# Optimization experiments

Hardware: AMD Instinct MI355X
Metric: run time of the kernel (lower is better)

Reference implementation:

```python
import jax, jax.numpy as jnp
import numpy as np

N = 131072       # total nodes (B graphs x P nodes)
P = 4096         # nodes per graph
B = 32           # graphs in batch
E = 2097152      # edges (avg degree 16)
IN_DIM = 64
HID = 128
OUT = 16
EPS = 1e-5
SLOPE = 0.01


def _degrees(idx):
    # structural degree, clamped to min 1 (as DGL GraphConv does)
    d = jax.ops.segment_sum(jnp.ones((E,), jnp.float32), idx, num_segments=N)
    return jnp.maximum(d, 1.0)


def _graph_conv(x, W, src, dst, ew):
    # DGL GraphConv, norm='both', bias=False, with scalar edge weights:
    # h = D_out^{-1/2} x ; m_v = sum_{(u->v)} w_e h_u ; out = (D_in^{-1/2} m) W
    h = x * jax.lax.rsqrt(_degrees(src))[:, None]
    m = jax.ops.segment_sum(ew[:, None] * h[src], dst, num_segments=N)  # [N, F]
    return (m * jax.lax.rsqrt(_degrees(dst))[:, None]) @ W


def _graph_norm(x, gamma, beta, alpha):
    # GraphNorm (Cai et al. / PyG, batch=None): stats over all nodes per feature
    mu = jnp.mean(x, axis=0)
    c = x - alpha * mu
    var = jnp.mean(c * c, axis=0)
    return c * jax.lax.rsqrt(var + EPS) * gamma + beta


def _mean_nodes(h, gid):
    # per-graph mean readout; every graph has exactly P nodes
    return jax.ops.segment_sum(h, gid, num_segments=B) / P


def setup_inputs() -> dict:
    key = jax.random.key(0)
    ks = jax.random.split(key, 8)
    src = jax.random.randint(ks[0], (E,), 0, N, dtype=jnp.int32)
    # keep edges within each 4096-node graph block (batched DGL graph)
    dst = (src // P) * P + jax.random.randint(ks[1], (E,), 0, P, dtype=jnp.int32)
    features = jax.random.normal(ks[2], (N, IN_DIM), jnp.float32)
    edge_weights = jax.random.uniform(ks[3], (E,), jnp.float32)
    # kaiming/xavier-scale init approximations
    W1 = jax.random.normal(ks[4], (IN_DIM, HID), jnp.float32) * np.sqrt(2.0 / IN_DIM)
    W2 = jax.random.normal(ks[5], (HID, HID), jnp.float32) * np.sqrt(2.0 / HID)
    Wc = jax.random.normal(ks[6], (OUT, 2 * HID), jnp.float32) * np.sqrt(1.0 / (2 * HID))
    ones = jnp.ones((HID,), jnp.float32)
    zeros = jnp.zeros((HID,), jnp.float32)
    return {
        'features': features, 'edge_weights': edge_weights, 'src': src, 'dst': dst,
        'W1': W1, 'W2': W2, 'Wc': Wc,
        'gamma1': ones, 'beta1': zeros, 'alpha1': ones,
        'gamma2': ones, 'beta2': zeros, 'alpha2': ones,
    }


def reference(features, edge_weights, src, dst, W1, W2, Wc,
              gamma1, beta1, alpha1, gamma2, beta2, alpha2):
    gid = jnp.arange(N, dtype=jnp.int32) // P  # node -> graph id
    h1 = _graph_conv(features, W1, src, dst, edge_weights)
    h1 = jax.nn.leaky_relu(_graph_norm(h1, gamma1, beta1, alpha1), SLOPE)
    r1 = _mean_nodes(h1, gid)                  # [B, HID]
    h2 = _graph_conv(h1, W2, src, dst, edge_weights)
    h2 = jax.nn.leaky_relu(_graph_norm(h2, gamma2, beta2, alpha2), SLOPE)
    r2 = _mean_nodes(h2, gid)                  # [B, HID]
    readouts = jnp.concatenate([r1, r2], axis=1)  # [B, 2*HID]
    return readouts @ Wc.T                     # [B, OUT]
```

## Files before the change

### kernel.cpp

```cpp
#include <hip/hip_runtime.h>
#include <hip/hip_fp16.h>

constexpr int NN   = 131072;
constexpr int PP   = 4096;
constexpr int BG   = 32;
constexpr int EE   = 2097152;
constexpr int IND  = 64;
constexpr int HH   = 128;
constexpr int CAP  = 69632;
constexpr float EPSV   = 1e-5f;
constexpr float SLOPEV = 0.01f;

typedef short bf16x8 __attribute__((ext_vector_type(8)));
typedef float f32x4  __attribute__((ext_vector_type(4)));

__device__ __forceinline__ unsigned f2bf(float f) {
    unsigned u = __float_as_uint(f);
    return (u + 0x7FFFu + ((u >> 16) & 1u)) >> 16;
}
__device__ __forceinline__ unsigned pack2bf(float lo, float hi) {
    return f2bf(lo) | (f2bf(hi) << 16);
}
__device__ __forceinline__ float bflo(unsigned p) { return __uint_as_float(p << 16); }
__device__ __forceinline__ float bfhi(unsigned p) { return __uint_as_float(p & 0xFFFF0000u); }
__device__ __forceinline__ float w16(unsigned r) {
    return __half2float(__ushort_as_half((unsigned short)(r >> 16)));
}

template <int K>
__device__ __forceinline__ void packw_body(const float* __restrict__ W,
                                           unsigned short* __restrict__ pw, int t) {
    if (t >= K * 16) return;
    int lane = t & 63, nt = (t >> 6) & 7, kt = t >> 9;
    int kbase = kt * 32 + ((lane >> 4) & 3) * 8;
    int col   = nt * 16 + (lane & 15);
    for (int j = 0; j < 8; j++)
        pw[t * 8 + j] = (unsigned short)f2bf(W[(kbase + j) * HH + col]);
}

__global__ __launch_bounds__(256) void k_prep(const float* __restrict__ features,
                                              unsigned* __restrict__ fx,
                                              const float* __restrict__ W1,
                                              unsigned short* __restrict__ pw1,
                                              const float* __restrict__ W2,
                                              unsigned short* __restrict__ pw2,
                                              int* __restrict__ gcur,
                                              float* __restrict__ racc) {
    int b = blockIdx.x, t = threadIdx.x;
    if (b < 16384) {
        int i = b * 256 + t;
        float2 v = ((const float2*)features)[i];
        fx[i] = pack2bf(v.x, v.y);
        return;
    }
    if (b == 16384) {
        if (t < BG) gcur[t * 16] = t * CAP;
        for (int i = t; i < 2 * BG * HH; i += 256) racc[i] = 0.f;
        return;
    }
    if (b < 16389) { packw_body<64>(W1, pw1, (b - 16385) * 256 + t); return; }
    packw_body<128>(W2, pw2, (b - 16389) * 256 + t);
}

__global__ __launch_bounds__(256) void k_part(const int* __restrict__ src,
                                              const int* __restrict__ dst,
                                              const float* __restrict__ ew,
                                              int* __restrict__ gcur,
                                              uint2* __restrict__ recs) {
    __shared__ int cnt[32];
    __shared__ int start[32];
    __shared__ int gbase[32];
    __shared__ uint2 stage[4096];
    int t = threadIdx.x;
    int ebase = blockIdx.x * 4096;
    if (t < 32) cnt[t] = 0;
    __syncthreads();
    int es[16]; int ed[16]; float ev[16];
#pragma unroll
    for (int k = 0; k < 16; k++) {
        int e = ebase + k * 256 + t;
        es[k] = src[e]; ed[k] = dst[e]; ev[k] = ew[e];
        atomicAdd(&cnt[es[k] >> 12], 1);
    }
    __syncthreads();
    if (t == 0) {
        int run = 0;
        for (int g = 0; g < 32; g++) { start[g] = run; run += cnt[g]; }
    }
    __syncthreads();
    if (t < 32) {
        gbase[t] = atomicAdd(&gcur[t * 16], cnt[t]);
        cnt[t] = start[t];
    }
    __syncthreads();
#pragma unroll
    for (int k = 0; k < 16; k++) {
        int g = es[k] >> 12;
        int pos = atomicAdd(&cnt[g], 1);
        stage[pos] = make_uint2((unsigned)(es[k] & 4095) | ((unsigned)(ed[k] & 4095) << 12) |
                                ((unsigned)g << 24), __float_as_uint(ev[k]));
    }
    __syncthreads();
    for (int i = t; i < 4096; i += 256) {
        uint2 r = stage[i];
        int g = r.x >> 24;
        recs[gbase[g] + (i - start[g])] = r;
    }
}

__global__ __launch_bounds__(1024) void k_hist(const uint2* __restrict__ recs,
                                               const int* __restrict__ gcur,
                                               int* __restrict__ shist,
                                               int* __restrict__ dhist) {
    __shared__ int hs[4096];
    __shared__ int hd[4096];
    int t = threadIdx.x;
    int g = blockIdx.x >> 3, c = blockIdx.x & 7;
    int n = gcur[g * 16] - g * CAP;
    int lo = (n * c) >> 3, hi = (n * (c + 1)) >> 3;
    ((int4*)hs)[t] = make_int4(0, 0, 0, 0);
    ((int4*)hd)[t] = make_int4(0, 0, 0, 0);
    __syncthreads();
    const uint2* base = recs + (size_t)g * CAP;
    for (int i = lo + t; i < hi; i += 1024) {
        unsigned x = base[i].x;
        atomicAdd(&hs[x & 4095], 1);
        atomicAdd(&hd[(x >> 12) & 4095], 1);
    }
    __syncthreads();
    ((int4*)(shist + (size_t)blockIdx.x * 4096))[t] = ((int4*)hs)[t];
    ((int4*)(dhist + (size_t)blockIdx.x * 4096))[t] = ((int4*)hd)[t];
}

__global__ __launch_bounds__(1024) void k_offs(int* __restrict__ shist,
                                               int* __restrict__ dhist,
                                               float* __restrict__ rs_s,
                                               float* __restrict__ rsd,
                                               int* __restrict__ degd,
                                               int* __restrict__ offs) {
    __shared__ int partial[1024];
    int t = threadIdx.x, g = blockIdx.x;
    int sdeg[4] = {0, 0, 0, 0}, ddeg[4] = {0, 0, 0, 0};
#pragma unroll
    for (int c = 0; c < 8; c++) {
        int4 sv = ((const int4*)(shist + (size_t)(g * 8 + c) * 4096))[t];
        int4 dv = ((const int4*)(dhist + (size_t)(g * 8 + c) * 4096))[t];
        sdeg[0] += sv.x; sdeg[1] += sv.y; sdeg[2] += sv.z; sdeg[3] += sv.w;
        ddeg[0] += dv.x; ddeg[1] += dv.y; ddeg[2] += dv.z; ddeg[3] += dv.w;
    }
#pragma unroll
    for (int j = 0; j < 4; j++) {
        int idx = t * 4 + j;
        int vs = sdeg[j]; if (vs < 1) vs = 1;
        rs_s[g * PP + idx] = rsqrtf((float)vs);
        int vd = ddeg[j]; if (vd < 1) vd = 1;
        rsd[g * PP + idx]  = rsqrtf((float)vd);
        degd[g * PP + idx] = ddeg[j];
    }
    partial[t] = ddeg[0] + ddeg[1] + ddeg[2] + ddeg[3];
    __syncthreads();
    for (int off = 1; off < 1024; off <<= 1) {
        int v = partial[t];
        int add = (t >= off) ? partial[t - off] : 0;
        __syncthreads();
        partial[t] = v + add;
        __syncthreads();
    }
    int run = (t == 0) ? 0 : partial[t - 1];
#pragma unroll
    for (int j = 0; j < 4; j++) {
        int idx = t * 4 + j;
        offs[g * PP + idx] = g * CAP + run;
        int nb = run;
        for (int c = 0; c < 8; c++) {
            size_t hidx = (size_t)(g * 8 + c) * 4096 + idx;
            int v = dhist[hidx];
            dhist[hidx] = nb;
            nb += v;
        }
        run = nb;
    }
}

__global__ __launch_bounds__(1024) void k_place(const uint2* __restrict__ recs,
                                                const int* __restrict__ gcur,
                                                const int* __restrict__ dhist,
                                                const float* __restrict__ rs_s,
                                                unsigned* __restrict__ csr2) {
    __shared__ int cur[4096];
    __shared__ float rss[4096];
    int t = threadIdx.x;
    int g = blockIdx.x >> 3, c = blockIdx.x & 7;
    int n = gcur[g * 16] - g * CAP;
    int lo = (n * c) >> 3, hi = (n * (c + 1)) >> 3;
    ((int4*)cur)[t] = ((const int4*)(dhist + (size_t)blockIdx.x * 4096))[t];
    ((float4*)rss)[t] = ((const float4*)(rs_s + (size_t)g * PP))[t];
    __syncthreads();
    const uint2* base = recs + (size_t)g * CAP;
    unsigned* cbase = csr2 + (size_t)g * CAP;
    for (int i = lo + t; i < hi; i += 1024) {
        uint2 r = base[i];
        int sl = r.x & 4095, dl = (r.x >> 12) & 4095;
        int pos = atomicAdd(&cur[dl], 1);
        float wf = __uint_as_float(r.y) * rss[sl];
        cbase[pos] = (unsigned)sl | ((unsigned)__half_as_ushort(__float2half(wf)) << 16);
    }
}

__global__ __launch_bounds__(256) void k_agg1(const unsigned* __restrict__ fx,
                                              const unsigned* __restrict__ csr2,
                                              const int* __restrict__ offs,
                                              const int* __restrict__ degd,
                                              const float* __restrict__ rsd,
                                              unsigned* __restrict__ m1) {
    int bid = blockIdx.x;
    int xcd = bid & 7, idx = bid >> 3;
    int g = xcd * 4 + (idx >> 9);
    int node0 = g * PP + (idx & 511) * 8;
    int lane = threadIdx.x & 63, wv = threadIdx.x >> 6;
    int half = lane >> 5, sl = lane & 31;
    int v = node0 + wv * 2 + half;
    int o = offs[v], cnt = degd[v];
    unsigned fb = (unsigned)(v & ~(PP - 1)) * 32;
    float ax0 = 0.f, ay0 = 0.f, ax1 = 0.f, ay1 = 0.f;
    int i = 0;
    for (; i + 4 <= cnt; i += 4) {
        unsigned r0 = csr2[o + i],     r1 = csr2[o + i + 1];
        unsigned r2 = csr2[o + i + 2], r3 = csr2[o + i + 3];
        unsigned g0 = fx[fb + (r0 & 4095) * 32 + sl];
        unsigned g1 = fx[fb + (r1 & 4095) * 32 + sl];
        unsigned g2 = fx[fb + (r2 & 4095) * 32 + sl];
        unsigned g3 = fx[fb + (r3 & 4095) * 32 + sl];
        float w0 = w16(r0), w1 = w16(r1), w2 = w16(r2), w3 = w16(r3);
        ax0 += w0 * bflo(g0); ay0 += w0 * bfhi(g0);
        ax1 += w1 * bflo(g1); ay1 += w1 * bfhi(g1);
        ax0 += w2 * bflo(g2); ay0 += w2 * bfhi(g2);
        ax1 += w3 * bflo(g3); ay1 += w3 * bfhi(g3);
    }
    for (; i < cnt; i++) {
        unsigned r = csr2[o + i];
        unsigned g0 = fx[fb + (r & 4095) * 32 + sl];
        float w = w16(r);
        ax0 += w * bflo(g0); ay0 += w * bfhi(g0);
    }
    float rd = rsd[v];
    m1[(size_t)v * 32 + sl] = pack2bf((ax0 + ax1) * rd, (ay0 + ay1) * rd);
}

__global__ __launch_bounds__(256) void k_agg2(const unsigned* __restrict__ h1,
                                              const unsigned* __restrict__ csr2,
                                              const int* __restrict__ offs,
                                              const int* __restrict__ degd,
                                              const float* __restrict__ rsd,
                                              unsigned* __restrict__ m2) {
    int bid = blockIdx.x;
    int xcd = bid & 7, idx = bid >> 3;
    int g = xcd * 4 + (idx >> 10);
    int node0 = g * PP + (idx & 1023) * 4;
    int lane = threadIdx.x & 63, wv = threadIdx.x >> 6;
    int v = node0 + wv;
    int o = offs[v], cnt = degd[v];
    unsigned hb = (unsigned)(v & ~(PP - 1)) * 64;
    float ax0 = 0.f, ay0 = 0.f, ax1 = 0.f, ay1 = 0.f;
    int i = 0;
    for (; i + 4 <= cnt; i += 4) {
        unsigned r0 = csr2[o + i],     r1 = csr2[o + i + 1];
        unsigned r2 = csr2[o + i + 2], r3 = csr2[o + i + 3];
        unsigned g0 = h1[hb + (r0 & 4095) * 64 + lane];
        unsigned g1 = h1[hb + (r1 & 4095) * 64 + lane];
        unsigned g2 = h1[hb + (r2 & 4095) * 64 + lane];
        unsigned g3 = h1[hb + (r3 & 4095) * 64 + lane];
        float w0 = w16(r0), w1 = w16(r1), w2 = w16(r2), w3 = w16(r3);
        ax0 += w0 * bflo(g0); ay0 += w0 * bfhi(g0);
        ax1 += w1 * bflo(g1); ay1 += w1 * bfhi(g1);
        ax0 += w2 * bflo(g2); ay0 += w2 * bfhi(g2);
        ax1 += w3 * bflo(g3); ay1 += w3 * bfhi(g3);
    }
    for (; i < cnt; i++) {
        unsigned r = csr2[o + i];
        unsigned g0 = h1[hb + (r & 4095) * 64 + lane];
        float w = w16(r);
        ax0 += w * bflo(g0); ay0 += w * bfhi(g0);
    }
    float rd = rsd[v];
    m2[(size_t)v * 64 + lane] = pack2bf((ax0 + ax1) * rd, (ay0 + ay1) * rd);
}

template <int K>
__global__ __launch_bounds__(256) void k_gemm(const short* __restrict__ A,
                                              const short* __restrict__ PW,
                                              unsigned short* __restrict__ C,
                                              float* __restrict__ part) {
    __shared__ float s1[HH], s2[HH];
    int t = threadIdx.x;
    if (t < HH) { s1[t] = 0.f; s2[t] = 0.f; }
    __syncthreads();
    int wv = t >> 6, lane = t & 63;
    int tile = blockIdx.x * 4 + wv;
    int m = lane & 15, quad = lane >> 4;
    int row = tile * 16 + m;
    bf16x8 a[K / 32];
#pragma unroll
    for (int kt = 0; kt < K / 32; kt++)
        a[kt] = *(const bf16x8*)(A + (size_t)row * K + kt * 32 + quad * 8);
#pragma unroll
    for (int nt = 0; nt < 8; nt++) {
        f32x4 acc = {0.f, 0.f, 0.f, 0.f};
#pragma unroll
        for (int kt = 0; kt < K / 32; kt++) {
            bf16x8 b = *(const bf16x8*)(PW + ((size_t)(kt * 8 + nt) * 64 + lane) * 8);
            acc = __builtin_amdgcn_mfma_f32_16x16x32_bf16(a[kt], b, acc, 0, 0, 0);
        }
        int col = nt * 16 + m;
        int r0 = tile * 16 + quad * 4;
        float ps = 0.f, pq = 0.f;
#pragma unroll
        for (int r = 0; r < 4; r++) {
            C[(size_t)(r0 + r) * HH + col] = (unsigned short)f2bf(acc[r]);
            ps += acc[r]; pq += acc[r] * acc[r];
        }
        atomicAdd(&s1[col], ps);
        atomicAdd(&s2[col], pq);
    }
    __syncthreads();
    if (t < HH) {
        part[blockIdx.x * 256 + t]      = s1[t];
        part[blockIdx.x * 256 + HH + t] = s2[t];
    }
}

__global__ __launch_bounds__(256) void k_red(const float* __restrict__ part,
                                             float* __restrict__ pb) {
    int t = threadIdx.x, b = blockIdx.x;
    float s = 0.f;
    for (int r = 0; r < 32; r++) s += part[(size_t)(b * 32 + r) * 256 + t];
    pb[b * 256 + t] = s;
}

__global__ void k_coef(const float* __restrict__ pb, const float* __restrict__ gamma,
                       const float* __restrict__ beta, const float* __restrict__ alpha,
                       float* __restrict__ ab) {
    int t = threadIdx.x;
    float s = 0.f;
    for (int b = 0; b < 64; b++) s += pb[b * 256 + t];
    __shared__ float sh[256];
    sh[t] = s;
    __syncthreads();
    if (t < 128) {
        float mu = sh[t] * (1.f / NN);
        float e2 = sh[128 + t] * (1.f / NN);
        float al = alpha[t];
        float var = e2 - (2.f * al - al * al) * mu * mu;
        float a = rsqrtf(var + EPSV) * gamma[t];
        ab[t] = a;
        ab[HH + t] = beta[t] - al * mu * a;
    }
}

template <bool WRITE>
__global__ __launch_bounds__(256) void k_normro(unsigned* __restrict__ h,
                                                const float* __restrict__ ab,
                                                float* __restrict__ racc) {
    int fp = threadIdx.x & 63;
    int q  = threadIdx.x >> 6;
    int node0 = blockIdx.x * 64;
    int g = node0 / PP;
    float a0 = ab[2 * fp], a1 = ab[2 * fp + 1];
    float b0 = ab[HH + 2 * fp], b1 = ab[HH + 2 * fp + 1];
    float s0 = 0.f, s1 = 0.f;
    for (int i = q; i < 64; i += 4) {
        size_t idx = (size_t)(node0 + i) * 64 + fp;
        unsigned v = h[idx];
        float x0 = fmaf(a0, bflo(v), b0); x0 = x0 > 0.f ? x0 : SLOPEV * x0;
        float x1 = fmaf(a1, bfhi(v), b1); x1 = x1 > 0.f ? x1 : SLOPEV * x1;
        if (WRITE) h[idx] = pack2bf(x0, x1);
        s0 += x0; s1 += x1;
    }
    __shared__ float sh[512];
    sh[threadIdx.x] = s0;
    sh[256 + threadIdx.x] = s1;
    __syncthreads();
    if (q == 0) {
        float t0 = s0 + sh[64 + fp] + sh[128 + fp] + sh[192 + fp];
        float t1 = s1 + sh[256 + 64 + fp] + sh[256 + 128 + fp] + sh[256 + 192 + fp];
        atomicAdd(&racc[g * HH + 2 * fp],     t0);
        atomicAdd(&racc[g * HH + 2 * fp + 1], t1);
    }
}

__global__ void k_final(const float* __restrict__ racc1, const float* __restrict__ racc2,
                        const float* __restrict__ Wc, float* __restrict__ out) {
    int t = threadIdx.x;
    int b = t >> 4, o = t & 15;
    float acc = 0.f;
    for (int f = 0; f < HH; f++) acc += racc1[b * HH + f] * Wc[o * (2 * HH) + f];
    for (int f = 0; f < HH; f++) acc += racc2[b * HH + f] * Wc[o * (2 * HH) + HH + f];
    out[t] = acc * (1.f / PP);
}

extern "C" void kernel_launch(void* const* d_in, const int* in_sizes, int n_in,
                              void* d_out, int out_size, void* d_ws, size_t ws_size,
                              hipStream_t stream) {
    const float* features = (const float*)d_in[0];
    const float* ew       = (const float*)d_in[1];
    const int*   src      = (const int*)d_in[2];
    const int*   dst      = (const int*)d_in[3];
    const float* W1       = (const float*)d_in[4];
    const float* W2       = (const float*)d_in[5];
    const float* Wc       = (const float*)d_in[6];
    const float* gamma1   = (const float*)d_in[7];
    const float* beta1    = (const float*)d_in[8];
    const float* alpha1   = (const float*)d_in[9];
    const float* gamma2   = (const float*)d_in[10];
    const float* beta2    = (const float*)d_in[11];
    const float* alpha2   = (const float*)d_in[12];
    float* out = (float*)d_out;

    char* w = (char*)d_ws;
    int*    gcur   = (int*)(w + 0);
    float*  racc1  = (float*)(w + (16u << 10));
    float*  racc2  = (float*)(w + (32u << 10));
    float*  ab1    = (float*)(w + (48u << 10));
    float*  ab2    = (float*)(w + (52u << 10));
    unsigned short* pw1 = (unsigned short*)(w + (64u << 10));
    unsigned short* pw2 = (unsigned short*)(w + (80u << 10));
    float*  pb     = (float*)(w + (128u << 10));
    float*  rs_s   = (float*)(w + (1024u << 10));
    float*  rsd    = (float*)(w + (1536u << 10));
    int*    degd   = (int*)(w + (2048u << 10));
    int*    offs   = (int*)(w + (2560u << 10));
    float*  part   = (float*)(w + (3u << 20));
    int*    shist  = (int*)(w + (5u << 20));
    int*    dhist  = (int*)(w + (9u << 20));
    unsigned* csr2 = (unsigned*)(w + (13u << 20));
    unsigned* mbuf = (unsigned*)(w + (22u << 20));
    unsigned* hbuf = (unsigned*)(w + (54u << 20));
    uint2*    recs = (uint2*)(w + (86u << 20));
    unsigned* fx   = (unsigned*)(w + (104u << 20));

    k_prep<<<16397, 256, 0, stream>>>(features, fx, W1, pw1, W2, pw2, gcur, racc1);

    k_part<<<EE / 4096, 256, 0, stream>>>(src, dst, ew, gcur, recs);
    k_hist<<<BG * 8, 1024, 0, stream>>>(recs, gcur, shist, dhist);
    k_offs<<<BG, 1024, 0, stream>>>(shist, dhist, rs_s, rsd, degd, offs);
    k_place<<<BG * 8, 1024, 0, stream>>>(recs, gcur, dhist, rs_s, csr2);

    k_agg1<<<NN / 8, 256, 0, stream>>>(fx, csr2, offs, degd, rsd, mbuf);
    k_gemm<64><<<NN / 64, 256, 0, stream>>>((const short*)mbuf, (const short*)pw1,
                                            (unsigned short*)hbuf, part);
    k_red<<<64, 256, 0, stream>>>(part, pb);
    k_coef<<<1, 256, 0, stream>>>(pb, gamma1, beta1, alpha1, ab1);
    k_normro<true><<<NN / 64, 256, 0, stream>>>(hbuf, ab1, racc1);

    k_agg2<<<NN / 4, 256, 0, stream>>>(hbuf, csr2, offs, degd, rsd, mbuf);
    k_gemm<128><<<NN / 64, 256, 0, stream>>>((const short*)mbuf, (const short*)pw2,
                                             (unsigned short*)hbuf, part);
    k_red<<<64, 256, 0, stream>>>(part, pb);
    k_coef<<<1, 256, 0, stream>>>(pb, gamma2, beta2, alpha2, ab2);
    k_normro<false><<<NN / 64, 256, 0, stream>>>(hbuf, ab2, racc2);

    k_final<<<1, 512, 0, stream>>>(racc1, racc2, Wc, out);
}
```

Measured before the change: 424.4 us.

## Split edges across wavefront lane groups with 8-byte gathers in aggregation kernels

Both aggregation kernels now assign one node per wavefront and split that node's edges across lane groups (4 groups in layer 1, 2 groups with 2 edges each in layer 2). Each lane loads 8-byte feature chunks instead of 4-byte ones, and partial sums are combined with cross-lane shuffles. The aim is fewer, wider gather instructions and more edges in flight per wave for the irregular feature reads. In exchange it adds shuffle reductions and a masked tail, half or three quarters of the lanes sit idle on the store, and layer 1 launches twice as many blocks.

```diff
diff --git a/kernel.cpp b/kernel.cpp
--- a/kernel.cpp
+++ b/kernel.cpp
@@ -215,36 +215,42 @@
                                               unsigned* __restrict__ m1) {
     int bid = blockIdx.x;
     int xcd = bid & 7, idx = bid >> 3;
-    int g = xcd * 4 + (idx >> 9);
-    int node0 = g * PP + (idx & 511) * 8;
+    int g = xcd * 4 + (idx >> 10);
+    int node0 = g * PP + (idx & 1023) * 4;
     int lane = threadIdx.x & 63, wv = threadIdx.x >> 6;
-    int half = lane >> 5, sl = lane & 31;
-    int v = node0 + wv * 2 + half;
+    int v = node0 + wv;
     int o = offs[v], cnt = degd[v];
-    unsigned fb = (unsigned)(v & ~(PP - 1)) * 32;
-    float ax0 = 0.f, ay0 = 0.f, ax1 = 0.f, ay1 = 0.f;
+    float rd = rsd[v];
+    int qi = lane >> 4, ql = lane & 15;
+    const unsigned* hp = fx + (size_t)((unsigned)(v & ~(PP - 1)) * 32) + ql * 2;
+    float a0 = 0.f, a1 = 0.f, a2 = 0.f, a3 = 0.f;
     int i = 0;
     for (; i + 4 <= cnt; i += 4) {
-        unsigned r0 = csr2[o + i],     r1 = csr2[o + i + 1];
-        unsigned r2 = csr2[o + i + 2], r3 = csr2[o + i + 3];
-        unsigned g0 = fx[fb + (r0 & 4095) * 32 + sl];
-        unsigned g1 = fx[fb + (r1 & 4095) * 32 + sl];
-        unsigned g2 = fx[fb + (r2 & 4095) * 32 + sl];
-        unsigned g3 = fx[fb + (r3 & 4095) * 32 + sl];
-        float w0 = w16(r0), w1 = w16(r1), w2 = w16(r2), w3 = w16(r3);
-        ax0 += w0 * bflo(g0); ay0 += w0 * bfhi(g0);
-        ax1 += w1 * bflo(g1); ay1 += w1 * bfhi(g1);
-        ax0 += w2 * bflo(g2); ay0 += w2 * bfhi(g2);
-        ax1 += w3 * bflo(g3); ay1 += w3 * bfhi(g3);
-    }
-    for (; i < cnt; i++) {
-        unsigned r = csr2[o + i];
-        unsigned g0 = fx[fb + (r & 4095) * 32 + sl];
+        unsigned r = csr2[o + i + qi];
         float w = w16(r);
-        ax0 += w * bflo(g0); ay0 += w * bfhi(g0);
-    }
-    float rd = rsd[v];
-    m1[(size_t)v * 32 + sl] = pack2bf((ax0 + ax1) * rd, (ay0 + ay1) * rd);
+        uint2 gg = *(const uint2*)(hp + (size_t)(r & 4095) * 32);
+        a0 += w * bflo(gg.x); a1 += w * bfhi(gg.x);
+        a2 += w * bflo(gg.y); a3 += w * bfhi(gg.y);
+    }
+    if (i < cnt) {
+        int j = i + qi;
+        bool valid = j < cnt;
+        unsigned r = csr2[valid ? o + j : o + i];
+        float w = valid ? w16(r) : 0.f;
+        uint2 gg = *(const uint2*)(hp + (size_t)(r & 4095) * 32);
+        a0 += w * bflo(gg.x); a1 += w * bfhi(gg.x);
+        a2 += w * bflo(gg.y); a3 += w * bfhi(gg.y);
+    }
+    a0 += __shfl_xor(a0, 16, 64); a0 += __shfl_xor(a0, 32, 64);
+    a1 += __shfl_xor(a1, 16, 64); a1 += __shfl_xor(a1, 32, 64);
+    a2 += __shfl_xor(a2, 16, 64); a2 += __shfl_xor(a2, 32, 64);
+    a3 += __shfl_xor(a3, 16, 64); a3 += __shfl_xor(a3, 32, 64);
+    if (qi == 0) {
+        uint2 ow;
+        ow.x = pack2bf(a0 * rd, a1 * rd);
+        ow.y = pack2bf(a2 * rd, a3 * rd);
+        *(uint2*)(m1 + (size_t)v * 32 + ql * 2) = ow;
+    }
 }
 
 __global__ __launch_bounds__(256) void k_agg2(const unsigned* __restrict__ h1,
@@ -260,30 +266,49 @@
     int lane = threadIdx.x & 63, wv = threadIdx.x >> 6;
     int v = node0 + wv;
     int o = offs[v], cnt = degd[v];
-    unsigned hb = (unsigned)(v & ~(PP - 1)) * 64;
-    float ax0 = 0.f, ay0 = 0.f, ax1 = 0.f, ay1 = 0.f;
+    float rd = rsd[v];
+    int half = lane >> 5, hl = lane & 31;
+    const unsigned* hp = h1 + (size_t)((unsigned)(v & ~(PP - 1)) * 64) + hl * 2;
+    float a0 = 0.f, a1 = 0.f, a2 = 0.f, a3 = 0.f;
+    float b0 = 0.f, b1 = 0.f, b2 = 0.f, b3 = 0.f;
     int i = 0;
     for (; i + 4 <= cnt; i += 4) {
-        unsigned r0 = csr2[o + i],     r1 = csr2[o + i + 1];
-        unsigned r2 = csr2[o + i + 2], r3 = csr2[o + i + 3];
-        unsigned g0 = h1[hb + (r0 & 4095) * 64 + lane];
-        unsigned g1 = h1[hb + (r1 & 4095) * 64 + lane];
-        unsigned g2 = h1[hb + (r2 & 4095) * 64 + lane];
-        unsigned g3 = h1[hb + (r3 & 4095) * 64 + lane];
-        float w0 = w16(r0), w1 = w16(r1), w2 = w16(r2), w3 = w16(r3);
-        ax0 += w0 * bflo(g0); ay0 += w0 * bfhi(g0);
-        ax1 += w1 * bflo(g1); ay1 += w1 * bfhi(g1);
-        ax0 += w2 * bflo(g2); ay0 += w2 * bfhi(g2);
-        ax1 += w3 * bflo(g3); ay1 += w3 * bfhi(g3);
-    }
-    for (; i < cnt; i++) {
-        unsigned r = csr2[o + i];
-        unsigned g0 = h1[hb + (r & 4095) * 64 + lane];
-        float w = w16(r);
-        ax0 += w * bflo(g0); ay0 += w * bfhi(g0);
-    }
-    float rd = rsd[v];
-    m2[(size_t)v * 64 + lane] = pack2bf((ax0 + ax1) * rd, (ay0 + ay1) * rd);
+        uint2 rr = *(const uint2*)(csr2 + o + i + half * 2);
+        float wa = w16(rr.x), wb = w16(rr.y);
+        uint2 ga = *(const uint2*)(hp + (size_t)(rr.x & 4095) * 64);
+        uint2 gb = *(const uint2*)(hp + (size_t)(rr.y & 4095) * 64);
+        a0 += wa * bflo(ga.x); a1 += wa * bfhi(ga.x);
+        a2 += wa * bflo(ga.y); a3 += wa * bfhi(ga.y);
+        b0 += wb * bflo(gb.x); b1 += wb * bfhi(gb.x);
+        b2 += wb * bflo(gb.y); b3 += wb * bfhi(gb.y);
+    }
+    if (i < cnt) {
+        int j = i + half;
+        bool v1 = j < cnt;
+        unsigned ra = csr2[v1 ? o + j : o + i];
+        float wa = v1 ? w16(ra) : 0.f;
+        uint2 ga = *(const uint2*)(hp + (size_t)(ra & 4095) * 64);
+        a0 += wa * bflo(ga.x); a1 += wa * bfhi(ga.x);
+        a2 += wa * bflo(ga.y); a3 += wa * bfhi(ga.y);
+        int j2 = j + 2;
+        bool v2 = j2 < cnt;
+        unsigned rb = csr2[v2 ? o + j2 : o + i];
+        float wb = v2 ? w16(rb) : 0.f;
+        uint2 gb = *(const uint2*)(hp + (size_t)(rb & 4095) * 64);
+        b0 += wb * bflo(gb.x); b1 += wb * bfhi(gb.x);
+        b2 += wb * bflo(gb.y); b3 += wb * bfhi(gb.y);
+    }
+    a0 += b0; a1 += b1; a2 += b2; a3 += b3;
+    a0 += __shfl_xor(a0, 32, 64);
+    a1 += __shfl_xor(a1, 32, 64);
+    a2 += __shfl_xor(a2, 32, 64);
+    a3 += __shfl_xor(a3, 32, 64);
+    if (half == 0) {
+        uint2 ow;
+        ow.x = pack2bf(a0 * rd, a1 * rd);
+        ow.y = pack2bf(a2 * rd, a3 * rd);
+        *(uint2*)(m2 + (size_t)v * 64 + hl * 2) = ow;
+    }
 }
 
 template <int K>
@@ -445,7 +470,7 @@
     k_offs<<<BG, 1024, 0, stream>>>(shist, dhist, rs_s, rsd, degd, offs);
     k_place<<<BG * 8, 1024, 0, stream>>>(recs, gcur, dhist, rs_s, csr2);
 
-    k_agg1<<<NN / 8, 256, 0, stream>>>(fx, csr2, offs, degd, rsd, mbuf);
+    k_agg1<<<NN / 4, 256, 0, stream>>>(fx, csr2, offs, degd, rsd, mbuf);
     k_gemm<64><<<NN / 64, 256, 0, stream>>>((const short*)mbuf, (const short*)pw1,
                                             (unsigned short*)hbuf, part);
     k_red<<<64, 256, 0, stream>>>(part, pb);
```

After: 445.7 us. 1.05x slower.

## Pad CSR rows to multiples of four and vectorize aggregation with two nodes per wave

Applied to the files above, without the earlier changes.

Each destination node's CSR segment is padded to a multiple of four entries, with zeroed padding so the extra entries carry weight zero. This lets both aggregation kernels read four packed edge records with one 16-byte load and drop the scalar tail loops. k_agg2 now processes two nodes per wavefront to get more gathers in flight and launches half as many blocks. The cost is a larger CSR capacity, a memset of the whole CSR buffer on every call, and some wasted gathers on padded entries.

```diff
diff --git a/kernel.cpp b/kernel.cpp
--- a/kernel.cpp
+++ b/kernel.cpp
@@ -7,7 +7,7 @@
 constexpr int EE   = 2097152;
 constexpr int IND  = 64;
 constexpr int HH   = 128;
-constexpr int CAP  = 69632;
+constexpr int CAP  = 81920;
 constexpr float EPSV   = 1e-5f;
 constexpr float SLOPEV = 0.01f;
 
@@ -148,6 +148,7 @@
         sdeg[0] += sv.x; sdeg[1] += sv.y; sdeg[2] += sv.z; sdeg[3] += sv.w;
         ddeg[0] += dv.x; ddeg[1] += dv.y; ddeg[2] += dv.z; ddeg[3] += dv.w;
     }
+    int pdeg[4];
 #pragma unroll
     for (int j = 0; j < 4; j++) {
         int idx = t * 4 + j;
@@ -155,9 +156,10 @@
         rs_s[g * PP + idx] = rsqrtf((float)vs);
         int vd = ddeg[j]; if (vd < 1) vd = 1;
         rsd[g * PP + idx]  = rsqrtf((float)vd);
-        degd[g * PP + idx] = ddeg[j];
-    }
-    partial[t] = ddeg[0] + ddeg[1] + ddeg[2] + ddeg[3];
+        pdeg[j] = (ddeg[j] + 3) & ~3;
+        degd[g * PP + idx] = pdeg[j];
+    }
+    partial[t] = pdeg[0] + pdeg[1] + pdeg[2] + pdeg[3];
     __syncthreads();
     for (int off = 1; off < 1024; off <<= 1) {
         int v = partial[t];
@@ -178,7 +180,7 @@
             dhist[hidx] = nb;
             nb += v;
         }
-        run = nb;
+        run += pdeg[j];
     }
 }
 
@@ -221,27 +223,19 @@
     int half = lane >> 5, sl = lane & 31;
     int v = node0 + wv * 2 + half;
     int o = offs[v], cnt = degd[v];
-    unsigned fb = (unsigned)(v & ~(PP - 1)) * 32;
+    const unsigned* hp = fx + (size_t)((unsigned)(g * PP) * 32) + sl;
     float ax0 = 0.f, ay0 = 0.f, ax1 = 0.f, ay1 = 0.f;
-    int i = 0;
-    for (; i + 4 <= cnt; i += 4) {
-        unsigned r0 = csr2[o + i],     r1 = csr2[o + i + 1];
-        unsigned r2 = csr2[o + i + 2], r3 = csr2[o + i + 3];
-        unsigned g0 = fx[fb + (r0 & 4095) * 32 + sl];
-        unsigned g1 = fx[fb + (r1 & 4095) * 32 + sl];
-        unsigned g2 = fx[fb + (r2 & 4095) * 32 + sl];
-        unsigned g3 = fx[fb + (r3 & 4095) * 32 + sl];
-        float w0 = w16(r0), w1 = w16(r1), w2 = w16(r2), w3 = w16(r3);
+    for (int i = 0; i < cnt; i += 4) {
+        uint4 rr = *(const uint4*)(csr2 + o + i);
+        unsigned g0 = hp[(rr.x & 4095) * 32];
+        unsigned g1 = hp[(rr.y & 4095) * 32];
+        unsigned g2 = hp[(rr.z & 4095) * 32];
+        unsigned g3 = hp[(rr.w & 4095) * 32];
+        float w0 = w16(rr.x), w1 = w16(rr.y), w2 = w16(rr.z), w3 = w16(rr.w);
         ax0 += w0 * bflo(g0); ay0 += w0 * bfhi(g0);
         ax1 += w1 * bflo(g1); ay1 += w1 * bfhi(g1);
         ax0 += w2 * bflo(g2); ay0 += w2 * bfhi(g2);
         ax1 += w3 * bflo(g3); ay1 += w3 * bfhi(g3);
-    }
-    for (; i < cnt; i++) {
-        unsigned r = csr2[o + i];
-        unsigned g0 = fx[fb + (r & 4095) * 32 + sl];
-        float w = w16(r);
-        ax0 += w * bflo(g0); ay0 += w * bfhi(g0);
     }
     float rd = rsd[v];
     m1[(size_t)v * 32 + sl] = pack2bf((ax0 + ax1) * rd, (ay0 + ay1) * rd);
@@ -255,35 +249,60 @@
                                               unsigned* __restrict__ m2) {
     int bid = blockIdx.x;
     int xcd = bid & 7, idx = bid >> 3;
-    int g = xcd * 4 + (idx >> 10);
-    int node0 = g * PP + (idx & 1023) * 4;
+    int g = xcd * 4 + (idx >> 9);
+    int node0 = g * PP + (idx & 511) * 4;
     int lane = threadIdx.x & 63, wv = threadIdx.x >> 6;
-    int v = node0 + wv;
-    int o = offs[v], cnt = degd[v];
-    unsigned hb = (unsigned)(v & ~(PP - 1)) * 64;
-    float ax0 = 0.f, ay0 = 0.f, ax1 = 0.f, ay1 = 0.f;
+    int va = node0 + wv, vb = va + 2048;
+    int oa = offs[va], ca = degd[va];
+    int ob = offs[vb], cb = degd[vb];
+    const unsigned* hp = h1 + (size_t)((unsigned)(g * PP) * 64) + lane;
+    float A0 = 0.f, A1 = 0.f, B0 = 0.f, B1 = 0.f;
+    int c0 = ca < cb ? ca : cb;
+    int cm = ca < cb ? cb : ca;
     int i = 0;
-    for (; i + 4 <= cnt; i += 4) {
-        unsigned r0 = csr2[o + i],     r1 = csr2[o + i + 1];
-        unsigned r2 = csr2[o + i + 2], r3 = csr2[o + i + 3];
-        unsigned g0 = h1[hb + (r0 & 4095) * 64 + lane];
-        unsigned g1 = h1[hb + (r1 & 4095) * 64 + lane];
-        unsigned g2 = h1[hb + (r2 & 4095) * 64 + lane];
-        unsigned g3 = h1[hb + (r3 & 4095) * 64 + lane];
-        float w0 = w16(r0), w1 = w16(r1), w2 = w16(r2), w3 = w16(r3);
-        ax0 += w0 * bflo(g0); ay0 += w0 * bfhi(g0);
-        ax1 += w1 * bflo(g1); ay1 += w1 * bfhi(g1);
-        ax0 += w2 * bflo(g2); ay0 += w2 * bfhi(g2);
-        ax1 += w3 * bflo(g3); ay1 += w3 * bfhi(g3);
-    }
-    for (; i < cnt; i++) {
-        unsigned r = csr2[o + i];
-        unsigned g0 = h1[hb + (r & 4095) * 64 + lane];
-        float w = w16(r);
-        ax0 += w * bflo(g0); ay0 += w * bfhi(g0);
-    }
-    float rd = rsd[v];
-    m2[(size_t)v * 64 + lane] = pack2bf((ax0 + ax1) * rd, (ay0 + ay1) * rd);
+    for (; i < c0; i += 4) {
+        uint4 ra = *(const uint4*)(csr2 + oa + i);
+        uint4 rb = *(const uint4*)(csr2 + ob + i);
+        unsigned ga0 = hp[(ra.x & 4095) * 64];
+        unsigned ga1 = hp[(ra.y & 4095) * 64];
+        unsigned ga2 = hp[(ra.z & 4095) * 64];
+        unsigned ga3 = hp[(ra.w & 4095) * 64];
+        unsigned gb0 = hp[(rb.x & 4095) * 64];
+        unsigned gb1 = hp[(rb.y & 4095) * 64];
+        unsigned gb2 = hp[(rb.z & 4095) * 64];
+        unsigned gb3 = hp[(rb.w & 4095) * 64];
+        float wa0 = w16(ra.x), wa1 = w16(ra.y), wa2 = w16(ra.z), wa3 = w16(ra.w);
+        float wb0 = w16(rb.x), wb1 = w16(rb.y), wb2 = w16(rb.z), wb3 = w16(rb.w);
+        A0 += wa0 * bflo(ga0); A1 += wa0 * bfhi(ga0);
+        A0 += wa1 * bflo(ga1); A1 += wa1 * bfhi(ga1);
+        A0 += wa2 * bflo(ga2); A1 += wa2 * bfhi(ga2);
+        A0 += wa3 * bflo(ga3); A1 += wa3 * bfhi(ga3);
+        B0 += wb0 * bflo(gb0); B1 += wb0 * bfhi(gb0);
+        B0 += wb1 * bflo(gb1); B1 += wb1 * bfhi(gb1);
+        B0 += wb2 * bflo(gb2); B1 += wb2 * bfhi(gb2);
+        B0 += wb3 * bflo(gb3); B1 += wb3 * bfhi(gb3);
+    }
+    if (i < cm) {
+        int ot = (ca > cb) ? oa : ob;
+        float E0 = 0.f, E1 = 0.f, F0 = 0.f, F1 = 0.f;
+        for (; i < cm; i += 4) {
+            uint4 rr = *(const uint4*)(csr2 + ot + i);
+            unsigned g0 = hp[(rr.x & 4095) * 64];
+            unsigned g1 = hp[(rr.y & 4095) * 64];
+            unsigned g2 = hp[(rr.z & 4095) * 64];
+            unsigned g3 = hp[(rr.w & 4095) * 64];
+            float w0 = w16(rr.x), w1 = w16(rr.y), w2 = w16(rr.z), w3 = w16(rr.w);
+            E0 += w0 * bflo(g0); E1 += w0 * bfhi(g0);
+            F0 += w1 * bflo(g1); F1 += w1 * bfhi(g1);
+            E0 += w2 * bflo(g2); E1 += w2 * bfhi(g2);
+            F0 += w3 * bflo(g3); F1 += w3 * bfhi(g3);
+        }
+        if (ca > cb) { A0 += E0 + F0; A1 += E1 + F1; }
+        else         { B0 += E0 + F0; B1 += E1 + F1; }
+    }
+    float rda = rsd[va], rdb = rsd[vb];
+    m2[(size_t)va * 64 + lane] = pack2bf(A0 * rda, A1 * rda);
+    m2[(size_t)vb * 64 + lane] = pack2bf(B0 * rdb, B1 * rdb);
 }
 
 template <int K>
@@ -433,12 +452,13 @@
     int*    shist  = (int*)(w + (5u << 20));
     int*    dhist  = (int*)(w + (9u << 20));
     unsigned* csr2 = (unsigned*)(w + (13u << 20));
-    unsigned* mbuf = (unsigned*)(w + (22u << 20));
-    unsigned* hbuf = (unsigned*)(w + (54u << 20));
-    uint2*    recs = (uint2*)(w + (86u << 20));
-    unsigned* fx   = (unsigned*)(w + (104u << 20));
+    unsigned* mbuf = (unsigned*)(w + (23u << 20));
+    unsigned* hbuf = (unsigned*)(w + (55u << 20));
+    uint2*    recs = (uint2*)(w + (87u << 20));
+    unsigned* fx   = (unsigned*)(w + (107u << 20));
 
     k_prep<<<16397, 256, 0, stream>>>(features, fx, W1, pw1, W2, pw2, gcur, racc1);
+    hipMemsetAsync(csr2, 0, (size_t)BG * CAP * sizeof(unsigned), stream);
 
     k_part<<<EE / 4096, 256, 0, stream>>>(src, dst, ew, gcur, recs);
     k_hist<<<BG * 8, 1024, 0, stream>>>(recs, gcur, shist, dhist);
@@ -452,7 +472,7 @@
     k_coef<<<1, 256, 0, stream>>>(pb, gamma1, beta1, alpha1, ab1);
     k_normro<true><<<NN / 64, 256, 0, stream>>>(hbuf, ab1, racc1);
 
-    k_agg2<<<NN / 4, 256, 0, stream>>>(hbuf, csr2, offs, degd, rsd, mbuf);
+    k_agg2<<<NN / 8, 256, 0, stream>>>(hbuf, csr2, offs, degd, rsd, mbuf);
     k_gemm<128><<<NN / 64, 256, 0, stream>>>((const short*)mbuf, (const short*)pw2,
                                              (unsigned short*)hbuf, part);
     k_red<<<64, 256, 0, stream>>>(part, pb);
```

Result: faster. 412.8 us (-2.7%).
